# Optimization experiments

Measured on AMD Instinct MI355X. Metric: run time of the kernel, lower is better.

Reference implementation:

```python
import jax, jax.numpy as jnp
import numpy as np


def setup_inputs() -> dict:
    key = jax.random.key(0)
    x = jax.random.normal(key, (4, 4, 32, 256, 256), dtype=jnp.float32)
    return {"x": x}


def reference(x):
    # NonMaximaSuppression3d with kernel_size=(3,3,3) fast path:
    # a voxel survives iff it is strictly greater than all 26 neighbors;
    # border voxels (no full neighborhood) are always suppressed.
    B, CH, D, H, W = x.shape
    ct = x[..., 1:-1, 1:-1, 1:-1]  # interior centers [B,CH,D-2,H-2,W-2]
    mask_inner = jnp.ones(ct.shape, dtype=bool)
    for dz in range(3):
        for dy in range(3):
            for dx in range(3):
                if (dz, dy, dx) == (1, 1, 1):
                    continue
                neigh = x[..., dz:D - 2 + dz, dy:H - 2 + dy, dx:W - 2 + dx]
                mask_inner = mask_inner & (ct > neigh)
    mask = jnp.zeros(x.shape, dtype=bool).at[..., 1:-1, 1:-1, 1:-1].set(mask_inner)
    return x * mask.astype(x.dtype)
```

## Files before the change

kernel.cpp:

```cpp
#include <hip/hip_runtime.h>


typedef float v4f __attribute__((ext_vector_type(4)));

constexpr int W  = 256;
constexpr int H  = 256;
constexpr int D  = 32;
constexpr int SH = W;
constexpr int SD = W * H;
constexpr int KD  = 4;
constexpr int HCW = 16;
constexpr int BC = 16;
constexpr int DG = D / KD;
constexpr int HG = H / HCW;
constexpr int NWG = BC * DG * HG;

__device__ __forceinline__ v4f vmax4(v4f a, v4f b) {
    return (v4f){fmaxf(a.x, b.x), fmaxf(a.y, b.y), fmaxf(a.z, b.z), fmaxf(a.w, b.w)};
}

__global__ __launch_bounds__(256, 4) void nms3d_kernel(const float* __restrict__ x,
                                                       float* __restrict__ out) {
    const int blk  = blockIdx.x;
    const int wv   = threadIdx.x >> 6;
    const int lane = threadIdx.x & 63;
    const int hg   = blk & (HG - 1);
    const int dg   = (blk >> 4) & (DG - 1);
    const int bc   = blk >> 7;
    const int d    = dg * KD + wv;
    const int h0   = hg * HCW;

    const float* vol = x + bc * (D * SD);
    const int pm = d == 0     ? 0     : d - 1;
    const int pp = d == D - 1 ? D - 1 : d + 1;
    const int om = pm * SD + (lane << 2);
    const int o0 = d  * SD + (lane << 2);
    const int op = pp * SD + (lane << 2);

    const bool dv = (d > 0) && (d < D - 1);
    float* ovol = out + bc * (D * SD) + d * SD + (lane << 2);

    v4f rm[4], r0[4], rp[4];

    #pragma unroll
    for (int r = 0; r < 3; ++r) {
        int hh = h0 - 1 + r; hh = hh < 0 ? 0 : hh;
        const int o = hh * SH;
        rm[r] = *(const v4f*)(vol + om + o);
        r0[r] = *(const v4f*)(vol + o0 + o);
        rp[r] = *(const v4f*)(vol + op + o);
    }

    #pragma unroll
    for (int i = 0; i < HCW; ++i) {
        if (i + 3 <= HCW + 1) {
            int hh = h0 - 1 + (i + 3); hh = hh > H - 1 ? H - 1 : hh;
            const int o = hh * SH, s = (i + 3) & 3;
            rm[s] = *(const v4f*)(vol + om + o);
            r0[s] = *(const v4f*)(vol + o0 + o);
            rp[s] = *(const v4f*)(vol + op + o);
        }
        const int s0 = i & 3, s1 = (i + 1) & 3, s2 = (i + 2) & 3;

        const v4f a3m = vmax4(vmax4(rm[s0], rm[s1]), rm[s2]);
        const v4f a3p = vmax4(vmax4(rp[s0], rp[s1]), rp[s2]);
        const v4f a20 = vmax4(r0[s0], r0[s2]);
        const v4f v8  = vmax4(vmax4(a3m, a3p), a20);
        const v4f c   = r0[s1];

        const float l8 = __shfl_up(v8.w, 1);
        const float r8 = __shfl_down(v8.x, 1);
        const float lc = __shfl_up(c.w, 1);
        const float rc = __shfl_down(c.x, 1);

        float n0 = fmaxf(fmaxf(l8,   v8.x), v8.y);
        float n1 = fmaxf(fmaxf(v8.x, v8.y), v8.z);
        float n2 = fmaxf(fmaxf(v8.y, v8.z), v8.w);
        float n3 = fmaxf(fmaxf(v8.z, v8.w), r8);
        n0 = fmaxf(n0, fmaxf(lc,  c.y));
        n1 = fmaxf(n1, fmaxf(c.x, c.z));
        n2 = fmaxf(n2, fmaxf(c.y, c.w));
        n3 = fmaxf(n3, fmaxf(c.z, rc));

        const int h = h0 + i;
        const bool hv = (h > 0) && (h < H - 1);
        const bool v  = hv && dv;
        v4f o;
        o.x = (v && lane > 0  && c.x > n0) ? c.x : 0.f;
        o.y = (v && c.y > n1) ? c.y : 0.f;
        o.z = (v && c.z > n2) ? c.z : 0.f;
        o.w = (v && lane < 63 && c.w > n3) ? c.w : 0.f;
        __builtin_nontemporal_store(o, (v4f*)(ovol + h * SH));
    }
}

extern "C" void kernel_launch(void* const* d_in, const int* in_sizes, int n_in,
                              void* d_out, int out_size, void* d_ws, size_t ws_size,
                              hipStream_t stream) {
    const float* x = (const float*)d_in[0];
    float* out = (float*)d_out;
    nms3d_kernel<<<NWG, 256, 0, stream>>>(x, out);
}
```

Baseline: 232.6 us.

## Stage halo rows through an LDS ring via async global_load_lds

Replaces the direct register loads of the three depth planes with asynchronous global-to-LDS loads into a 4-entry ring per wave. Explicit vmcnt waits and sched barriers pipeline these loads, and each row is then read back from LDS into a 3-slot register window. The aim is to hide global memory latency and cut the register footprint of the prefetch buffer. In exchange, each block uses about 48KB of LDS, launch bounds drop to 3 blocks per CU, and correctness relies on the hand-written vmcnt counts.

```diff
diff --git a/kernel.cpp b/kernel.cpp
--- a/kernel.cpp
+++ b/kernel.cpp
@@ -10,17 +10,38 @@
 constexpr int SD = W * H;
 constexpr int KD  = 4;
 constexpr int HCW = 16;
-constexpr int BC = 16;
-constexpr int DG = D / KD;
-constexpr int HG = H / HCW;
+constexpr int BC  = 16;
+constexpr int DG  = D / KD;
+constexpr int HG  = H / HCW;
 constexpr int NWG = BC * DG * HG;
+constexpr int EF  = 3 * W;
+constexpr int RF  = 4 * EF;
 
 __device__ __forceinline__ v4f vmax4(v4f a, v4f b) {
     return (v4f){fmaxf(a.x, b.x), fmaxf(a.y, b.y), fmaxf(a.z, b.z), fmaxf(a.w, b.w)};
 }
 
-__global__ __launch_bounds__(256, 4) void nms3d_kernel(const float* __restrict__ x,
+__device__ __forceinline__ void stage_entry(const float* __restrict__ vol,
+                                            float* ring, int j, int h0,
+                                            int om, int o0, int op) {
+    int hh = h0 - 1 + j; hh = hh < 0 ? 0 : (hh > H - 1 ? H - 1 : hh);
+    const int ro = hh * SH;
+    float* dst = ring + (j & 3) * EF;
+    __builtin_amdgcn_global_load_lds(
+        (const __attribute__((address_space(1))) unsigned int*)(vol + om + ro),
+        (__attribute__((address_space(3))) unsigned int*)(dst + 0 * W), 16, 0, 0);
+    __builtin_amdgcn_global_load_lds(
+        (const __attribute__((address_space(1))) unsigned int*)(vol + o0 + ro),
+        (__attribute__((address_space(3))) unsigned int*)(dst + 1 * W), 16, 0, 0);
+    __builtin_amdgcn_global_load_lds(
+        (const __attribute__((address_space(1))) unsigned int*)(vol + op + ro),
+        (__attribute__((address_space(3))) unsigned int*)(dst + 2 * W), 16, 0, 0);
+}
+
+__global__ __launch_bounds__(256, 3) void nms3d_kernel(const float* __restrict__ x,
                                                        float* __restrict__ out) {
+    __shared__ float lds[4 * RF];
+
     const int blk  = blockIdx.x;
     const int wv   = threadIdx.x >> 6;
     const int lane = threadIdx.x & 63;
@@ -39,34 +60,49 @@
 
     const bool dv = (d > 0) && (d < D - 1);
     float* ovol = out + bc * (D * SD) + d * SD + (lane << 2);
+    float* ring = lds + wv * RF;
+    const float* cring = ring + (lane << 2);
 
-    v4f rm[4], r0[4], rp[4];
+    stage_entry(vol, ring, 0, h0, om, o0, op);
+    stage_entry(vol, ring, 1, h0, om, o0, op);
+    stage_entry(vol, ring, 2, h0, om, o0, op);
 
-    #pragma unroll
-    for (int r = 0; r < 3; ++r) {
-        int hh = h0 - 1 + r; hh = hh < 0 ? 0 : hh;
-        const int o = hh * SH;
-        rm[r] = *(const v4f*)(vol + om + o);
-        r0[r] = *(const v4f*)(vol + o0 + o);
-        rp[r] = *(const v4f*)(vol + op + o);
-    }
+    v4f wm[3], w0[3], wp[3];
 
     #pragma unroll
     for (int i = 0; i < HCW; ++i) {
-        if (i + 3 <= HCW + 1) {
-            int hh = h0 - 1 + (i + 3); hh = hh > H - 1 ? H - 1 : hh;
-            const int o = hh * SH, s = (i + 3) & 3;
-            rm[s] = *(const v4f*)(vol + om + o);
-            r0[s] = *(const v4f*)(vol + o0 + o);
-            rp[s] = *(const v4f*)(vol + op + o);
+        if (i + 3 <= HCW + 1)
+            stage_entry(vol, ring, i + 3, h0, om, o0, op);
+        __builtin_amdgcn_sched_barrier(0);
+
+        if (i == 0)            asm volatile("s_waitcnt vmcnt(3)" ::: "memory");
+        else if (i + 3 <= HCW + 1) asm volatile("s_waitcnt vmcnt(4)" ::: "memory");
+        else                   asm volatile("s_waitcnt vmcnt(1)" ::: "memory");
+        __builtin_amdgcn_sched_barrier(0);
+
+        if (i == 0) {
+            #pragma unroll
+            for (int j = 0; j < 3; ++j) {
+                const float* e = cring + (j & 3) * EF;
+                wm[j] = *(const v4f*)(e + 0 * W);
+                w0[j] = *(const v4f*)(e + 1 * W);
+                wp[j] = *(const v4f*)(e + 2 * W);
+            }
+        } else {
+            const int j = i + 2, s = j % 3;
+            const float* e = cring + (j & 3) * EF;
+            wm[s] = *(const v4f*)(e + 0 * W);
+            w0[s] = *(const v4f*)(e + 1 * W);
+            wp[s] = *(const v4f*)(e + 2 * W);
         }
-        const int s0 = i & 3, s1 = (i + 1) & 3, s2 = (i + 2) & 3;
 
-        const v4f a3m = vmax4(vmax4(rm[s0], rm[s1]), rm[s2]);
-        const v4f a3p = vmax4(vmax4(rp[s0], rp[s1]), rp[s2]);
-        const v4f a20 = vmax4(r0[s0], r0[s2]);
+        const int a = i % 3, b = (i + 1) % 3, cc = (i + 2) % 3;
+
+        const v4f a3m = vmax4(vmax4(wm[a], wm[b]), wm[cc]);
+        const v4f a3p = vmax4(vmax4(wp[a], wp[b]), wp[cc]);
+        const v4f a20 = vmax4(w0[a], w0[cc]);
         const v4f v8  = vmax4(vmax4(a3m, a3p), a20);
-        const v4f c   = r0[s1];
+        const v4f c   = w0[b];
 
         const float l8 = __shfl_up(v8.w, 1);
         const float r8 = __shfl_down(v8.x, 1);
```

Measured after the change: 231.7 us. Within noise of the previous version (-0.4%).
